# Kernel tuning notes

Hardware: AMD Instinct MI355X
Metric: run time of the kernel (lower is better)

The kernel has to match this reference:

```python
import jax, jax.numpy as jnp
import numpy as np

N = 50000
E = 800000
D = 64
EPS = 1e-12
NEG_SLOPE = 0.01


def sage_conv(x, edge_index, W_l, b_l, W_r):
    """PyG SAGEConv (aggr='mean', root_weight=True):
    out = mean_{j in N(i)} x_j @ W_l^T + b_l + x_i @ W_r^T
    """
    src, dst = edge_index[0], edge_index[1]
    n = x.shape[0]
    # gather messages from source nodes, scatter-add into destination nodes
    sums = jax.ops.segment_sum(x[src], dst, num_segments=n)            # [N, D]
    cnt = jax.ops.segment_sum(jnp.ones((src.shape[0],), x.dtype), dst,
                              num_segments=n)                          # [N]
    mean = sums / jnp.maximum(cnt, 1.0)[:, None]                       # [N, D]
    return mean @ W_l.T + b_l + x @ W_r.T


def setup_inputs() -> dict:
    key = jax.random.key(0)
    k = jax.random.split(key, 8)
    x = jax.random.normal(k[0], (N, D), dtype=jnp.float32)
    edge_index = jax.random.randint(k[1], (2, E), 0, N, dtype=jnp.int64)
    edge_weight = jax.random.uniform(k[2], (E,), dtype=jnp.float32)
    s1 = 1.0 / np.sqrt(D)
    W1_l = jax.random.uniform(k[3], (D, D), minval=-s1, maxval=s1, dtype=jnp.float32)
    W1_r = jax.random.uniform(k[4], (D, D), minval=-s1, maxval=s1, dtype=jnp.float32)
    b1 = jnp.zeros((D,), jnp.float32)
    W2_l = jax.random.uniform(k[5], (D, D), minval=-s1, maxval=s1, dtype=jnp.float32)
    W2_r = jax.random.uniform(k[6], (D, D), minval=-s1, maxval=s1, dtype=jnp.float32)
    b2 = jnp.zeros((D,), jnp.float32)
    return {"x": x, "edge_index": edge_index, "edge_weight": edge_weight,
            "W1_l": W1_l, "b1": b1, "W1_r": W1_r,
            "W2_l": W2_l, "b2": b2, "W2_r": W2_r}


def reference(x, edge_index, edge_weight, W1_l, b1, W1_r, W2_l, b2, W2_r):
    # edge_weight is accepted for signature fidelity but SAGEConv ignores it.
    h = sage_conv(x, edge_index, W1_l, b1, W1_r)
    h = jnp.where(h >= 0, h, NEG_SLOPE * h)        # leaky_relu(0.01)
    # dropout -> identity (deterministic inference baseline)
    h = sage_conv(h, edge_index, W2_l, b2, W2_r)
    # F.normalize(p=2, dim=1, eps=1e-12)
    norm = jnp.maximum(jnp.linalg.norm(h, axis=1, keepdims=True), EPS)
    return h / norm
```

## Files before the change

### kernel.cpp

```cpp
#include <hip/hip_runtime.h>

#define DIM 64

typedef __bf16 bf16x8 __attribute__((ext_vector_type(8)));
typedef float f32x4 __attribute__((ext_vector_type(4)));

__device__ __forceinline__ unsigned short f2bf(float f) {
  unsigned u = __float_as_uint(f);
  u += 0x7fffu + ((u >> 16) & 1u);
  return (unsigned short)(u >> 16);
}
__device__ __forceinline__ float bflo(unsigned v) { return __uint_as_float(v << 16); }
__device__ __forceinline__ float bfhi(unsigned v) { return __uint_as_float(v & 0xffff0000u); }

__device__ __forceinline__ uint4 pack8(float4 a, float4 b) {
  uint4 o;
  o.x = ((unsigned)f2bf(a.y) << 16) | f2bf(a.x);
  o.y = ((unsigned)f2bf(a.w) << 16) | f2bf(a.z);
  o.z = ((unsigned)f2bf(b.y) << 16) | f2bf(b.x);
  o.w = ((unsigned)f2bf(b.w) << 16) | f2bf(b.z);
  return o;
}
__device__ __forceinline__ bf16x8 u4bf(uint4 u) {
  union { uint4 u4; bf16x8 b; } c;
  c.u4 = u;
  return c.b;
}

__global__ __launch_bounds__(256) void cvt_hist_kernel(
    const float* __restrict__ in, unsigned short* __restrict__ outb, int total8,
    const int4* __restrict__ dst4, int* __restrict__ deg, int E4) {
  int i = blockIdx.x * 256 + threadIdx.x;
  if (i < total8) {
    const float4* p = (const float4*)in + 2 * (size_t)i;
    ((uint4*)outb)[i] = pack8(p[0], p[1]);
  }
  if (i < E4) {
    int4 d = dst4[i];
    atomicAdd(&deg[d.x], 1);
    atomicAdd(&deg[d.y], 1);
    atomicAdd(&deg[d.z], 1);
    atomicAdd(&deg[d.w], 1);
  }
}

__global__ __launch_bounds__(256) void scan1_kernel(const int* __restrict__ deg,
                                                    int* __restrict__ rowptr,
                                                    int* __restrict__ bsum, int n) {
  __shared__ int sm[256];
  const int t = threadIdx.x, i = blockIdx.x * 256 + t;
  int v = (i < n) ? deg[i] : 0;
  sm[t] = v;
  __syncthreads();
  for (int off = 1; off < 256; off <<= 1) {
    int u = (t >= off) ? sm[t - off] : 0;
    __syncthreads();
    sm[t] += u;
    __syncthreads();
  }
  if (i < n) rowptr[i] = sm[t] - v;
  if (t == 255) bsum[blockIdx.x] = sm[255];
}

__global__ __launch_bounds__(1024) void scan2_kernel(const int* __restrict__ bsum,
                                                     int* __restrict__ bofs,
                                                     int* __restrict__ rowptr,
                                                     int nb, int n) {
  __shared__ int sm[1024];
  const int t = threadIdx.x;
  int v = (t < nb) ? bsum[t] : 0;
  sm[t] = v;
  __syncthreads();
  for (int off = 1; off < 1024; off <<= 1) {
    int u = (t >= off) ? sm[t - off] : 0;
    __syncthreads();
    sm[t] += u;
    __syncthreads();
  }
  if (t < nb) bofs[t] = sm[t] - v;
  if (t == 1023) rowptr[n] = sm[1023];
}

__global__ __launch_bounds__(256) void scan3_kernel(int* __restrict__ rowptr,
                                                    int* __restrict__ cursor,
                                                    const int* __restrict__ bofs,
                                                    int n) {
  int i = blockIdx.x * 256 + threadIdx.x;
  if (i < n) {
    int r = rowptr[i] + bofs[blockIdx.x];
    rowptr[i] = r;
    cursor[i] = r;
  }
}

__global__ __launch_bounds__(256) void fill_kernel(
    const int* __restrict__ src, const int* __restrict__ dst,
    int* __restrict__ cursor, unsigned short* __restrict__ eidx, int E) {
  int i = blockIdx.x * 256 + threadIdx.x;
  if (i >= E) return;
  int p = atomicAdd(&cursor[dst[i]], 1);
  eidx[p] = (unsigned short)src[i];
}

__global__ __launch_bounds__(256) void gather_kernel(
    const unsigned short* __restrict__ fb, const int* __restrict__ rowptr,
    const unsigned short* __restrict__ eidx, unsigned short* __restrict__ meanb,
    int n) {
  const int node = (blockIdx.x * 256 + threadIdx.x) >> 6;
  if (node >= n) return;
  const int l = threadIdx.x & 63;
  const int lane32 = l & 31;
  const int r0 = rowptr[node], r1 = rowptr[node + 1];
  float a0 = 0.f, a1 = 0.f, b0 = 0.f, b1 = 0.f;
  float c0 = 0.f, c1 = 0.f, d0 = 0.f, d1 = 0.f;
  int k = r0 + (l >> 5);
  for (; k + 8 <= r1; k += 8) {
    int s0 = eidx[k], s1 = eidx[k + 2], s2 = eidx[k + 4], s3 = eidx[k + 6];
    unsigned v0 = *(const unsigned*)&fb[(size_t)s0 * DIM + 2 * lane32];
    unsigned v1 = *(const unsigned*)&fb[(size_t)s1 * DIM + 2 * lane32];
    unsigned v2 = *(const unsigned*)&fb[(size_t)s2 * DIM + 2 * lane32];
    unsigned v3 = *(const unsigned*)&fb[(size_t)s3 * DIM + 2 * lane32];
    a0 += bflo(v0); a1 += bfhi(v0);
    b0 += bflo(v1); b1 += bfhi(v1);
    c0 += bflo(v2); c1 += bfhi(v2);
    d0 += bflo(v3); d1 += bfhi(v3);
  }
  for (; k < r1; k += 2) {
    unsigned v = *(const unsigned*)&fb[(size_t)eidx[k] * DIM + 2 * lane32];
    a0 += bflo(v);
    a1 += bfhi(v);
  }
  a0 = (a0 + b0) + (c0 + d0);
  a1 = (a1 + b1) + (c1 + d1);
  a0 += __shfl_xor(a0, 32, 64);
  a1 += __shfl_xor(a1, 32, 64);
  if (l < 32) {
    const int deg = r1 - r0;
    const float inv = deg ? 1.0f / (float)deg : 0.0f;
    unsigned pk = ((unsigned)f2bf(a1 * inv) << 16) | f2bf(a0 * inv);
    *(unsigned*)&meanb[(size_t)node * DIM + 2 * l] = pk;
  }
}

__global__ __launch_bounds__(256) void megagemm_kernel(
    const unsigned short* __restrict__ meanb, const unsigned short* __restrict__ xb,
    const float* __restrict__ W1l, const float* __restrict__ b1,
    const float* __restrict__ W1r, const float* __restrict__ W2l,
    const float* __restrict__ b2, const float* __restrict__ W2r,
    unsigned short* __restrict__ hlb, float* __restrict__ hr, int n) {
  __shared__ unsigned short w1l_b[4096];
  __shared__ unsigned short w1r_b[4096];
  __shared__ unsigned short w2l_b[4096];
  __shared__ unsigned short w2r_b[4096];
  __shared__ unsigned short h_b[4096];
  const int tid = threadIdx.x;
  const int base = blockIdx.x * 64;

#pragma unroll
  for (int j = 0; j < 2; ++j) {
    int sl = tid + j * 256;
    int row = sl >> 3, s = sl & 7;
    int dst = row * 64 + ((s ^ (row & 7)) << 3);
    const float4* p;
    p = (const float4*)W1l + 2 * sl;
    *(uint4*)&w1l_b[dst] = pack8(p[0], p[1]);
    p = (const float4*)W1r + 2 * sl;
    *(uint4*)&w1r_b[dst] = pack8(p[0], p[1]);
    p = (const float4*)W2l + 2 * sl;
    *(uint4*)&w2l_b[dst] = pack8(p[0], p[1]);
    p = (const float4*)W2r + 2 * sl;
    *(uint4*)&w2r_b[dst] = pack8(p[0], p[1]);
  }
  __syncthreads();

  const int w = tid >> 6;
  const int lane = tid & 63;
  const int lo = lane & 15;
  const int kg = lane >> 4;

  f32x4 acc[4];
#pragma unroll
  for (int i = 0; i < 4; ++i) acc[i] = (f32x4){0.f, 0.f, 0.f, 0.f};

#pragma unroll
  for (int kc = 0; kc < 4; ++kc) {
    const int col = (kc & 1) * 32 + kg * 8;
    const unsigned short* srcA = (kc < 2) ? meanb : xb;
    int rg = base + 16 * w + lo;
    if (rg > n - 1) rg = n - 1;
    bf16x8 af = u4bf(*(const uint4*)&srcA[(size_t)rg * DIM + col]);
    const unsigned short* wb = (kc < 2) ? w1l_b : w1r_b;
#pragma unroll
    for (int nb = 0; nb < 4; ++nb) {
      const int nr = 16 * nb + lo;
      bf16x8 bfr = u4bf(*(const uint4*)&wb[nr * 64 + (((col >> 3) ^ (nr & 7)) << 3)]);
      acc[nb] = __builtin_amdgcn_mfma_f32_16x16x32_bf16(af, bfr, acc[nb], 0, 0, 0);
    }
  }

#pragma unroll
  for (int nb = 0; nb < 4; ++nb) {
    const int nr = 16 * nb + lo;
    const float bb = b1[nr];
#pragma unroll
    for (int r = 0; r < 4; ++r) {
      float v = acc[nb][r] + bb;
      v = v >= 0.f ? v : 0.01f * v;
      const int m = 16 * w + kg * 4 + r;
      h_b[m * 64 + (((nr >> 3) ^ (m & 7)) << 3) + (nr & 7)] = f2bf(v);
    }
  }

  f32x4 dq[4], eq[4];
#pragma unroll
  for (int i = 0; i < 4; ++i) {
    dq[i] = (f32x4){0.f, 0.f, 0.f, 0.f};
    eq[i] = (f32x4){0.f, 0.f, 0.f, 0.f};
  }
#pragma unroll
  for (int kc = 0; kc < 2; ++kc) {
    const int col = kc * 32 + kg * 8;
    const int m = 16 * w + lo;
    bf16x8 af = u4bf(*(const uint4*)&h_b[m * 64 + (((col >> 3) ^ (m & 7)) << 3)]);
#pragma unroll
    for (int nb = 0; nb < 4; ++nb) {
      const int nr = 16 * nb + lo;
      const int ws = ((col >> 3) ^ (nr & 7)) << 3;
      bf16x8 bl = u4bf(*(const uint4*)&w2l_b[nr * 64 + ws]);
      bf16x8 br = u4bf(*(const uint4*)&w2r_b[nr * 64 + ws]);
      dq[nb] = __builtin_amdgcn_mfma_f32_16x16x32_bf16(af, bl, dq[nb], 0, 0, 0);
      eq[nb] = __builtin_amdgcn_mfma_f32_16x16x32_bf16(af, br, eq[nb], 0, 0, 0);
    }
  }

#pragma unroll
  for (int nb = 0; nb < 4; ++nb) {
    const int nr = 16 * nb + lo;
    const float bb = b2[nr];
#pragma unroll
    for (int r = 0; r < 4; ++r) {
      const int node = base + 16 * w + kg * 4 + r;
      if (node < n) {
        hlb[(size_t)node * DIM + nr] = f2bf(dq[nb][r]);
        hr[(size_t)node * DIM + nr] = eq[nb][r] + bb;
      }
    }
  }
}

__global__ __launch_bounds__(256) void gather_norm_kernel(
    const unsigned short* __restrict__ hlb, const int* __restrict__ rowptr,
    const unsigned short* __restrict__ eidx, const float* __restrict__ hr,
    float* __restrict__ out, int n) {
  const int node = (blockIdx.x * 256 + threadIdx.x) >> 6;
  if (node >= n) return;
  const int l = threadIdx.x & 63;
  const int lane32 = l & 31;
  const int r0 = rowptr[node], r1 = rowptr[node + 1];
  float a0 = 0.f, a1 = 0.f, b0 = 0.f, b1 = 0.f;
  float c0 = 0.f, c1 = 0.f, d0 = 0.f, d1 = 0.f;
  int k = r0 + (l >> 5);
  for (; k + 8 <= r1; k += 8) {
    int s0 = eidx[k], s1 = eidx[k + 2], s2 = eidx[k + 4], s3 = eidx[k + 6];
    unsigned v0 = *(const unsigned*)&hlb[(size_t)s0 * DIM + 2 * lane32];
    unsigned v1 = *(const unsigned*)&hlb[(size_t)s1 * DIM + 2 * lane32];
    unsigned v2 = *(const unsigned*)&hlb[(size_t)s2 * DIM + 2 * lane32];
    unsigned v3 = *(const unsigned*)&hlb[(size_t)s3 * DIM + 2 * lane32];
    a0 += bflo(v0); a1 += bfhi(v0);
    b0 += bflo(v1); b1 += bfhi(v1);
    c0 += bflo(v2); c1 += bfhi(v2);
    d0 += bflo(v3); d1 += bfhi(v3);
  }
  for (; k < r1; k += 2) {
    unsigned v = *(const unsigned*)&hlb[(size_t)eidx[k] * DIM + 2 * lane32];
    a0 += bflo(v);
    a1 += bfhi(v);
  }
  a0 = (a0 + b0) + (c0 + d0);
  a1 = (a1 + b1) + (c1 + d1);
  a0 += __shfl_xor(a0, 32, 64);
  a1 += __shfl_xor(a1, 32, 64);
  if (l < 32) {
    const int deg = r1 - r0;
    const float inv = deg ? 1.0f / (float)deg : 0.0f;
    float2 hv = *(const float2*)&hr[(size_t)node * DIM + 2 * lane32];
    float v0 = a0 * inv + hv.x;
    float v1 = a1 * inv + hv.y;
    float s = v0 * v0 + v1 * v1;
    s += __shfl_xor(s, 1, 32);
    s += __shfl_xor(s, 2, 32);
    s += __shfl_xor(s, 4, 32);
    s += __shfl_xor(s, 8, 32);
    s += __shfl_xor(s, 16, 32);
    float sc = 1.0f / fmaxf(sqrtf(s), 1e-12f);
    float2 o;
    o.x = v0 * sc;
    o.y = v1 * sc;
    *(float2*)&out[(size_t)node * DIM + 2 * lane32] = o;
  }
}

extern "C" void kernel_launch(void* const* d_in, const int* in_sizes, int n_in,
                              void* d_out, int out_size, void* d_ws,
                              size_t ws_size, hipStream_t stream) {
  const float* x = (const float*)d_in[0];
  const int* ei = (const int*)d_in[1];
  const float* W1l = (const float*)d_in[3];
  const float* b1 = (const float*)d_in[4];
  const float* W1r = (const float*)d_in[5];
  const float* W2l = (const float*)d_in[6];
  const float* b2 = (const float*)d_in[7];
  const float* W2r = (const float*)d_in[8];

  const int n = in_sizes[0] / DIM;
  const int E = in_sizes[1] / 2;
  const int* src = ei;
  const int* dst = ei + E;

  int* deg = (int*)d_ws;
  int* rowptr = deg + n;
  int* cursor = rowptr + n + 1;
  int* bsum = cursor + n;
  int* bofs = bsum + 1024;
  unsigned short* eidx = (unsigned short*)(bofs + 1024);
  size_t off = (size_t)3 * n + 1 + 2048 + (E + 1) / 2;
  off = (off + 3) & ~(size_t)3;
  unsigned short* meanb = (unsigned short*)((int*)d_ws + off);
  unsigned short* hlb = meanb + (size_t)n * DIM;
  float* hr = (float*)(hlb + (size_t)n * DIM);
  unsigned short* fbuf = (unsigned short*)(hr + (size_t)n * DIM);
  float* out = (float*)d_out;

  hipMemsetAsync(deg, 0, (size_t)n * sizeof(int), stream);

  const int E4 = E / 4;
  const int total8 = n * (DIM / 8);
  const int fb = (max(total8, E4) + 255) / 256;
  const int eb = (E + 255) / 256;
  const int nb1 = (n + 255) / 256;
  const int gb = (n + 3) / 4;
  const int mb = (n + 63) / 64;

  cvt_hist_kernel<<<fb, 256, 0, stream>>>(x, fbuf, total8, (const int4*)dst,
                                          deg, E4);
  scan1_kernel<<<nb1, 256, 0, stream>>>(deg, rowptr, bsum, n);
  scan2_kernel<<<1, 1024, 0, stream>>>(bsum, bofs, rowptr, nb1, n);
  scan3_kernel<<<nb1, 256, 0, stream>>>(rowptr, cursor, bofs, n);
  fill_kernel<<<eb, 256, 0, stream>>>(src, dst, cursor, eidx, E);

  gather_kernel<<<gb, 256, 0, stream>>>(fbuf, rowptr, eidx, meanb, n);
  megagemm_kernel<<<mb, 256, 0, stream>>>(meanb, fbuf, W1l, b1, W1r, W2l, b2,
                                          W2r, hlb, hr, n);
  gather_norm_kernel<<<gb, 256, 0, stream>>>(hlb, rowptr, eidx, hr, out, n);
}
```

Measured before the change: 241.3 us.

## Record per-edge rank during histogram to remove fill-stage atomics

The degree histogram now keeps the value returned by each atomicAdd as the edge's rank within its destination row and stores it as a ushort. The CSR fill kernel then computes each slot as rowptr[dst] + rank with plain stores, so it no longer needs 800K atomics on a cursor array. The fill kernel is also vectorized to four edges per thread. The cost is an extra rank buffer written and read back (about 1.6 MB). It also assumes no node has more than 65535 incoming edges, and it drops the cursor copy in scan3.

```diff
diff --git a/kernel.cpp b/kernel.cpp
--- a/kernel.cpp
+++ b/kernel.cpp
@@ -29,7 +29,8 @@
 
 __global__ __launch_bounds__(256) void cvt_hist_kernel(
     const float* __restrict__ in, unsigned short* __restrict__ outb, int total8,
-    const int4* __restrict__ dst4, int* __restrict__ deg, int E4) {
+    const int4* __restrict__ dst4, int* __restrict__ deg,
+    ushort4* __restrict__ rank4, int E4) {
   int i = blockIdx.x * 256 + threadIdx.x;
   if (i < total8) {
     const float4* p = (const float4*)in + 2 * (size_t)i;
@@ -37,10 +38,12 @@
   }
   if (i < E4) {
     int4 d = dst4[i];
-    atomicAdd(&deg[d.x], 1);
-    atomicAdd(&deg[d.y], 1);
-    atomicAdd(&deg[d.z], 1);
-    atomicAdd(&deg[d.w], 1);
+    ushort4 r;
+    r.x = (unsigned short)atomicAdd(&deg[d.x], 1);
+    r.y = (unsigned short)atomicAdd(&deg[d.y], 1);
+    r.z = (unsigned short)atomicAdd(&deg[d.z], 1);
+    r.w = (unsigned short)atomicAdd(&deg[d.w], 1);
+    rank4[i] = r;
   }
 }
 
@@ -82,24 +85,25 @@
 }
 
 __global__ __launch_bounds__(256) void scan3_kernel(int* __restrict__ rowptr,
-                                                    int* __restrict__ cursor,
                                                     const int* __restrict__ bofs,
                                                     int n) {
   int i = blockIdx.x * 256 + threadIdx.x;
-  if (i < n) {
-    int r = rowptr[i] + bofs[blockIdx.x];
-    rowptr[i] = r;
-    cursor[i] = r;
-  }
+  if (i < n) rowptr[i] += bofs[blockIdx.x];
 }
 
 __global__ __launch_bounds__(256) void fill_kernel(
-    const int* __restrict__ src, const int* __restrict__ dst,
-    int* __restrict__ cursor, unsigned short* __restrict__ eidx, int E) {
+    const int4* __restrict__ src4, const int4* __restrict__ dst4,
+    const ushort4* __restrict__ rank4, const int* __restrict__ rowptr,
+    unsigned short* __restrict__ eidx, int E4) {
   int i = blockIdx.x * 256 + threadIdx.x;
-  if (i >= E) return;
-  int p = atomicAdd(&cursor[dst[i]], 1);
-  eidx[p] = (unsigned short)src[i];
+  if (i >= E4) return;
+  int4 s = src4[i];
+  int4 d = dst4[i];
+  ushort4 r = rank4[i];
+  eidx[rowptr[d.x] + r.x] = (unsigned short)s.x;
+  eidx[rowptr[d.y] + r.y] = (unsigned short)s.y;
+  eidx[rowptr[d.z] + r.z] = (unsigned short)s.z;
+  eidx[rowptr[d.w] + r.w] = (unsigned short)s.w;
 }
 
 __global__ __launch_bounds__(256) void gather_kernel(
@@ -319,16 +323,24 @@
 
   int* deg = (int*)d_ws;
   int* rowptr = deg + n;
-  int* cursor = rowptr + n + 1;
-  int* bsum = cursor + n;
+  size_t o = (size_t)n + n + 1;
+  o = (o + 1) & ~(size_t)1;
+  int* bsum = (int*)d_ws + o;
   int* bofs = bsum + 1024;
-  unsigned short* eidx = (unsigned short*)(bofs + 1024);
-  size_t off = (size_t)3 * n + 1 + 2048 + (E + 1) / 2;
-  off = (off + 3) & ~(size_t)3;
-  unsigned short* meanb = (unsigned short*)((int*)d_ws + off);
-  unsigned short* hlb = meanb + (size_t)n * DIM;
-  float* hr = (float*)(hlb + (size_t)n * DIM);
-  unsigned short* fbuf = (unsigned short*)(hr + (size_t)n * DIM);
+  o += 2048;
+  unsigned short* rank = (unsigned short*)((int*)d_ws + o);
+  o += (E + 1) / 2;
+  o = (o + 1) & ~(size_t)1;
+  unsigned short* eidx = (unsigned short*)((int*)d_ws + o);
+  o += (E + 1) / 2;
+  o = (o + 3) & ~(size_t)3;
+  unsigned short* meanb = (unsigned short*)((int*)d_ws + o);
+  o += (size_t)n * (DIM / 2);
+  unsigned short* hlb = (unsigned short*)((int*)d_ws + o);
+  o += (size_t)n * (DIM / 2);
+  float* hr = (float*)((int*)d_ws + o);
+  o += (size_t)n * DIM;
+  unsigned short* fbuf = (unsigned short*)((int*)d_ws + o);
   float* out = (float*)d_out;
 
   hipMemsetAsync(deg, 0, (size_t)n * sizeof(int), stream);
@@ -336,17 +348,18 @@
   const int E4 = E / 4;
   const int total8 = n * (DIM / 8);
   const int fb = (max(total8, E4) + 255) / 256;
-  const int eb = (E + 255) / 256;
+  const int eb4 = (E4 + 255) / 256;
   const int nb1 = (n + 255) / 256;
   const int gb = (n + 3) / 4;
   const int mb = (n + 63) / 64;
 
   cvt_hist_kernel<<<fb, 256, 0, stream>>>(x, fbuf, total8, (const int4*)dst,
-                                          deg, E4);
+                                          deg, (ushort4*)rank, E4);
   scan1_kernel<<<nb1, 256, 0, stream>>>(deg, rowptr, bsum, n);
   scan2_kernel<<<1, 1024, 0, stream>>>(bsum, bofs, rowptr, nb1, n);
-  scan3_kernel<<<nb1, 256, 0, stream>>>(rowptr, cursor, bofs, n);
-  fill_kernel<<<eb, 256, 0, stream>>>(src, dst, cursor, eidx, E);
+  scan3_kernel<<<nb1, 256, 0, stream>>>(rowptr, bofs, n);
+  fill_kernel<<<eb4, 256, 0, stream>>>((const int4*)src, (const int4*)dst,
+                                       (const ushort4*)rank, rowptr, eidx, E4);
 
   gather_kernel<<<gb, 256, 0, stream>>>(fbuf, rowptr, eidx, meanb, n);
   megagemm_kernel<<<mb, 256, 0, stream>>>(meanb, fbuf, W1l, b1, W1r, W2l, b2,
```

Result: faster. 211.8 us (-12.2%).
